# Kernel tuning notes

Measured on AMD Instinct MI355X. Metric: run time of the kernel, lower is better.

Reference implementation:

```python
import jax, jax.numpy as jnp
import numpy as np

COMMITMENT_COST = 0.25
NUM_CODES = 4096
EMBED_DIM = 64


def setup_inputs() -> dict:
    key = jax.random.key(0)
    k1, k2 = jax.random.split(key)
    z_e = jax.random.normal(k1, (65536, EMBED_DIM), dtype=jnp.float32)
    embeddings = jax.random.normal(k2, (NUM_CODES, EMBED_DIM), dtype=jnp.float32)
    return {"z_e": z_e, "embeddings": embeddings}


def reference(z_e, embeddings):
    # Squared Euclidean distances; argmin is identical to torch.cdist argmin.
    # d2[n,k] = |z_e[n]|^2 - 2 z_e[n].e[k] + |e[k]|^2
    z_sq = jnp.sum(z_e * z_e, axis=-1, keepdims=True)            # [N,1]
    e_sq = jnp.sum(embeddings * embeddings, axis=-1)              # [K]
    d2 = z_sq - 2.0 * jnp.einsum('nd,kd->nk', z_e, embeddings) + e_sq  # [N,K]
    indices = jnp.argmin(d2, axis=-1)                             # [N] int
    z_q = embeddings[indices]                                     # [N,D] gather

    # commitment loss = mse(stop_grad(z_q), z_e)
    commitment_loss = COMMITMENT_COST * jnp.mean(
        (jax.lax.stop_gradient(z_q) - z_e) ** 2)

    # straight-through estimator
    z_q_st = z_e + jax.lax.stop_gradient(z_q - z_e)

    # code usage stats: one-hot mean == normalized histogram (scatter-add)
    n = z_e.shape[0]
    counts = jnp.zeros((NUM_CODES,), dtype=jnp.float32).at[indices].add(1.0)
    avg_probs = counts / n
    perplexity = jnp.exp(-jnp.sum(avg_probs * jnp.log(avg_probs + 1e-10)))
    n_active = jnp.sum(avg_probs > 0.001)

    return z_q_st, indices, commitment_loss, perplexity, n_active
```

## Files before the change

### kernel.cpp

```cpp
#include <hip/hip_runtime.h>
#include <math.h>

#define D 64
#define K 4096
#define MARGIN 0.08f
#define KSPLIT 4
#define CPH (K / 16 / KSPLIT)

typedef float f32x4 __attribute__((ext_vector_type(4)));
typedef _Float16 f16x8 __attribute__((ext_vector_type(8)));

__global__ __launch_bounds__(256) void esplit_kernel(const float* __restrict__ emb,
                                                     short* __restrict__ e_h,
                                                     float* __restrict__ e_sq,
                                                     int* __restrict__ counts,
                                                     int* __restrict__ ctrl) {
  int i = blockIdx.x * 256 + threadIdx.x;
  {
    int lane = i & 63;
    int t = (i >> 6) & 1;
    int c = i >> 7;
    int quad = lane >> 4, col = lane & 15;
    const float* src = emb + (size_t)(c * 16 + col) * D + t * 32 + quad * 8;
    f32x4 u0 = *(const f32x4*)src;
    f32x4 u1 = *(const f32x4*)(src + 4);
    f16x8 h;
#pragma unroll
    for (int j = 0; j < 8; ++j) {
      float x = (j < 4) ? u0[j] : u1[j - 4];
      h[j] = (_Float16)x;
    }
    *(f16x8*)(e_h + (size_t)i * 8) = h;
  }
  if (i < 128) ctrl[i] = 0;
  if (i < K) {
    counts[i] = 0;
    const float* e = emb + (size_t)i * D;
    float s = 0.f;
#pragma unroll
    for (int d = 0; d < D; ++d) s = fmaf(e[d], e[d], s);
    e_sq[i] = s;
  }
}

#define MFMA16(A, B, C) __builtin_amdgcn_mfma_f32_16x16x32_f16(A, B, C, 0, 0, 0)

#define STEP(C0, C1, CEQ, N0, N1, NEQ, CC)                                   \
  {                                                                          \
    N0 = *(const f16x8*)(pB);                                                \
    N1 = *(const f16x8*)(pB + 512);                                          \
    NEQ = *pE;                                                               \
    pB += 1024;                                                              \
    pE += 16;                                                                \
    const float seed = -0.5f * (CEQ);                                        \
    f32x4 acc0 = {seed, seed, seed, seed};                                   \
    f32x4 acc1 = {seed, seed, seed, seed};                                   \
    acc0 = MFMA16(a_hi[0][0], C0, acc0);                                     \
    acc1 = MFMA16(a_hi[1][0], C0, acc1);                                     \
    acc0 = MFMA16(a_lo[0][0], C0, acc0);                                     \
    acc1 = MFMA16(a_lo[1][0], C0, acc1);                                     \
    acc0 = MFMA16(a_hi[0][1], C1, acc0);                                     \
    acc1 = MFMA16(a_hi[1][1], C1, acc1);                                     \
    acc0 = MFMA16(a_lo[0][1], C1, acc0);                                     \
    acc1 = MFMA16(a_lo[1][1], C1, acc1);                                     \
    const int cc_ = (CC);                                                    \
    _Pragma("unroll")                                                        \
    for (int r = 0; r < 4; ++r) {                                            \
      float a0 = acc0[r];                                                    \
      float ob = best[r];                                                    \
      best[r] = fmaxf(ob, a0);                                               \
      second[r] = __builtin_amdgcn_fmed3f(ob, a0, second[r]);                \
      bidx[r] = (a0 > ob) ? cc_ : bidx[r];                                   \
    }                                                                        \
    _Pragma("unroll")                                                        \
    for (int r = 0; r < 4; ++r) {                                            \
      float a1 = acc1[r];                                                    \
      float ob = best[4 + r];                                                \
      best[4 + r] = fmaxf(ob, a1);                                           \
      second[4 + r] = __builtin_amdgcn_fmed3f(ob, a1, second[4 + r]);        \
      bidx[4 + r] = (a1 > ob) ? cc_ : bidx[4 + r];                           \
    }                                                                        \
  }

__global__ __launch_bounds__(256, 2) void dist_kernel(const float* __restrict__ z_e,
                                                      const short* __restrict__ e_h,
                                                      const float* __restrict__ esq,
                                                      float* __restrict__ pbest,
                                                      float* __restrict__ psec,
                                                      int* __restrict__ pidx) {
  const int tid = threadIdx.x;
  const int wv = tid >> 6;
  const int lane = tid & 63;
  const int quad = lane >> 4, col = lane & 15;
  const int rowbase = blockIdx.x * 128 + wv * 32;
  const int half = blockIdx.y;
  const int c0 = half * CPH;

  f16x8 a_hi[2][2], a_lo[2][2];
#pragma unroll
  for (int s = 0; s < 2; ++s) {
#pragma unroll
    for (int t = 0; t < 2; ++t) {
      const float* zr = z_e + (size_t)(rowbase + s * 16 + col) * D + t * 32 + quad * 8;
      f32x4 u0 = *(const f32x4*)zr;
      f32x4 u1 = *(const f32x4*)(zr + 4);
#pragma unroll
      for (int j = 0; j < 8; ++j) {
        float x = (j < 4) ? u0[j] : u1[j - 4];
        _Float16 h = (_Float16)x;
        a_hi[s][t][j] = h;
        a_lo[s][t][j] = (_Float16)(x - (float)h);
      }
    }
  }

  float best[8], second[8];
  int bidx[8];
#pragma unroll
  for (int i = 0; i < 8; ++i) {
    best[i] = -__builtin_inff();
    second[i] = -__builtin_inff();
    bidx[i] = 0;
  }

  const short* pB = e_h + (size_t)c0 * 1024 + (size_t)lane * 8;
  const float* pE = esq + c0 * 16 + col;
  f16x8 b0 = *(const f16x8*)pB;
  f16x8 b1 = *(const f16x8*)(pB + 512);
  float eq = *pE;
  pB += 1024;
  pE += 16;
  f16x8 n0, n1;
  float neq;

  for (int cc = 0; cc < CPH; cc += 2) {
    STEP(b0, b1, eq, n0, n1, neq, cc)
    STEP(n0, n1, neq, b0, b1, eq, cc + 1)
  }

#pragma unroll
  for (int i = 0; i < 8; ++i) {
    float b = -2.f * best[i];
    float s2 = -2.f * second[i];
    int ix = (c0 + bidx[i]) * 16 + col;
#pragma unroll
    for (int off = 1; off < 16; off <<= 1) {
      float ob = __shfl_xor(b, off);
      float os = __shfl_xor(s2, off);
      int oi = __shfl_xor(ix, off);
      float ns = fminf(fminf(s2, os), fmaxf(b, ob));
      if (ob < b || (ob == b && oi < ix)) ix = oi;
      b = fminf(b, ob);
      s2 = ns;
    }
    if (col == 0) {
      int row = rowbase + (i >> 2) * 16 + quad * 4 + (i & 3);
      size_t o = (size_t)half * 65536 + row;
      pbest[o] = b;
      psec[o] = s2;
      pidx[o] = ix;
    }
  }
}

__global__ __launch_bounds__(256) void tail_kernel(const float* __restrict__ z_e,
                                                   const float* __restrict__ emb,
                                                   const float* __restrict__ esq,
                                                   const float* __restrict__ pbest,
                                                   const float* __restrict__ psec,
                                                   const int* __restrict__ pidx,
                                                   float* __restrict__ out_zq,
                                                   float* __restrict__ out_idx,
                                                   int* __restrict__ counts,
                                                   int* __restrict__ ctrl,
                                                   float* __restrict__ out_scalars,
                                                   int N) {
  const int tid = threadIdx.x;
  const int wave = tid >> 6;
  const int lane = tid & 63;
  const int base = blockIdx.x * 128;
  int* done = ctrl;
  float* loss_slots = (float*)(ctrl + 8);

  __shared__ int wl[128];
  __shared__ int bidx_s[128];
  __shared__ int wn;
  __shared__ int lastflag;
  __shared__ float zs[4][D];
  __shared__ float se[4];
  __shared__ int sa[4];

  if (tid == 0) wn = 0;
  __syncthreads();

  if (tid < 128) {
    int row = base + tid;
    float b = pbest[row];
    float s2 = psec[row];
    int ix = pidx[row];
#pragma unroll
    for (int h = 1; h < KSPLIT; ++h) {
      size_t o = (size_t)h * 65536 + row;
      float bh = pbest[o];
      float sh = psec[o];
      int ih = pidx[o];
      s2 = fminf(fminf(s2, sh), fmaxf(b, bh));
      if (bh < b) ix = ih;
      b = fminf(b, bh);
    }
    bidx_s[tid] = ix;
    if (s2 - b < MARGIN) {
      int slot = atomicAdd(&wn, 1);
      wl[slot] = row;
    }
  }
  __syncthreads();

  const int n = wn;
  for (int j = wave; j < n; j += 4) {
    const int row = wl[j];
    if (lane < 16) ((f32x4*)zs[wave])[lane] = *((const f32x4*)(z_e + (size_t)row * D) + lane);

    float pb[KSPLIT], ps[KSPLIT];
    int pi[KSPLIT];
    float B = __builtin_inff();
#pragma unroll
    for (int h = 0; h < KSPLIT; ++h) {
      size_t o = (size_t)h * 65536 + row;
      pb[h] = pbest[o];
      ps[h] = psec[o];
      pi[h] = pidx[o];
      B = fminf(B, pb[h]);
    }
    const float lim = B + MARGIN;

    float bv = __builtin_inff();
    int bi = 0;
#pragma unroll
    for (int h = 0; h < KSPLIT; ++h) {
      if (ps[h] < lim) {
        float hb = __builtin_inff();
        int hx = 0;
        for (int t = 0; t < 16; ++t) {
          int c = h * 1024 + t * 64 + lane;
          const f32x4* er = (const f32x4*)(emb + (size_t)c * D);
          f32x4 a = {0.f, 0.f, 0.f, 0.f};
#pragma unroll
          for (int i = 0; i < 16; ++i)
            a = __builtin_elementwise_fma(er[i], ((const f32x4*)zs[wave])[i], a);
          float dot = (a[0] + a[1]) + (a[2] + a[3]);
          float q = fmaf(-2.f, dot, esq[c]);
          if (q < hb) { hb = q; hx = c; }
        }
#pragma unroll
        for (int off = 32; off > 0; off >>= 1) {
          float ov = __shfl_down(hb, off);
          int oi = __shfl_down(hx, off);
          if (ov < hb || (ov == hb && oi < hx)) { hb = ov; hx = oi; }
        }
        hb = __shfl(hb, 0);
        hx = __shfl(hx, 0);
        if (hb < bv || (hb == bv && hx < bi)) { bv = hb; bi = hx; }
      } else if (pb[h] < lim) {
        int c = pi[h];
        float p = emb[(size_t)c * D + lane] * zs[wave][lane];
#pragma unroll
        for (int off = 1; off < 64; off <<= 1) p += __shfl_xor(p, off);
        float q = fmaf(-2.f, p, esq[c]);
        if (q < bv || (q == bv && c < bi)) { bv = q; bi = c; }
      }
    }
    if (lane == 0) bidx_s[row - base] = bi;
  }
  __syncthreads();

  float lloss = 0.f;
  for (int r = wave; r < 128; r += 8) {
    const int r1 = r + 4;
    const int i0 = bidx_s[r];
    const int i1 = bidx_s[r1];
    const size_t row0 = base + r, row1 = base + r1;
    float ze0 = z_e[row0 * D + lane];
    float ze1 = z_e[row1 * D + lane];
    float zq0 = emb[(size_t)i0 * D + lane];
    float zq1 = emb[(size_t)i1 * D + lane];
    out_zq[row0 * D + lane] = ze0 + (zq0 - ze0);
    out_zq[row1 * D + lane] = ze1 + (zq1 - ze1);
    float d0 = zq0 - ze0, d1 = zq1 - ze1;
    lloss = fmaf(d0, d0, lloss);
    lloss = fmaf(d1, d1, lloss);
    if (lane == 0) {
      out_idx[row0] = (float)i0;
      out_idx[row1] = (float)i1;
      atomicAdd(&counts[i0], 1);
      atomicAdd(&counts[i1], 1);
    }
  }
#pragma unroll
  for (int off = 32; off > 0; off >>= 1) lloss += __shfl_down(lloss, off);
  if (lane == 0) atomicAdd(&loss_slots[blockIdx.x & 63], lloss);

  __syncthreads();
  if (tid == 0) {
    __threadfence();
    lastflag = (atomicAdd(done, 1) == (int)gridDim.x - 1);
  }
  __syncthreads();
  if (!lastflag) return;

  float ent = 0.f;
  int act = 0;
  const float invN = 1.0f / (float)N;
  for (int k = tid; k < K; k += 256) {
    float p = (float)atomicAdd(&counts[k], 0) * invN;
    ent += p * logf(p + 1e-10f);
    act += (p > 0.001f) ? 1 : 0;
  }
#pragma unroll
  for (int off = 32; off > 0; off >>= 1) {
    ent += __shfl_down(ent, off);
    act += __shfl_down(act, off);
  }
  if (lane == 0) { se[wave] = ent; sa[wave] = act; }

  float L = 0.f;
  if (wave == 0) {
    L = atomicAdd(&loss_slots[lane], 0.f);
#pragma unroll
    for (int off = 32; off > 0; off >>= 1) L += __shfl_down(L, off);
  }
  __syncthreads();
  if (tid == 0) {
    float E = se[0] + se[1] + se[2] + se[3];
    int A = sa[0] + sa[1] + sa[2] + sa[3];
    out_scalars[0] = 0.25f * L / ((float)N * (float)D);
    out_scalars[1] = expf(-E);
    out_scalars[2] = (float)A;
  }
}

extern "C" void kernel_launch(void* const* d_in, const int* in_sizes, int n_in,
                              void* d_out, int out_size, void* d_ws, size_t ws_size,
                              hipStream_t stream) {
  const float* z_e = (const float*)d_in[0];
  const float* emb = (const float*)d_in[1];
  const int N = in_sizes[0] / D;

  float* out = (float*)d_out;
  float* out_zq = out;
  float* out_idx = out + (size_t)N * D;
  float* out_scalars = out + (size_t)N * (D + 1);

  char* ws = (char*)d_ws;
  size_t o = 0;
  int* counts = (int*)(ws + o);      o += 16384;
  int* ctrl = (int*)(ws + o);        o += 512;
  float* esq = (float*)(ws + o);     o += 16384;
  short* e_h = (short*)(ws + o);     o += (size_t)K * D * 2;
  o += 8192;
  float* pbest = (float*)(ws + o);   o += (size_t)KSPLIT * N * 4;
  float* psec = (float*)(ws + o);    o += (size_t)KSPLIT * N * 4;
  int* pidx = (int*)(ws + o);        o += (size_t)KSPLIT * N * 4;

  esplit_kernel<<<(K / 16) * 2 * 64 / 256, 256, 0, stream>>>(emb, e_h, esq,
                                                             counts, ctrl);
  dist_kernel<<<dim3(N / 128, KSPLIT), 256, 0, stream>>>(z_e, e_h, esq,
                                                         pbest, psec, pidx);
  tail_kernel<<<N / 128, 256, 0, stream>>>(z_e, emb, esq, pbest, psec, pidx,
                                           out_zq, out_idx, counts, ctrl,
                                           out_scalars, N);
}
```

Measured before the change: 235.6 us.

## Stage codebook tiles in LDS with double-buffered global_load_lds

Each wave used to stream its own copy of the fp16 codebook fragments straight from global memory with register prefetch. Now the four waves of a block share a double-buffered LDS tile of 8 code chunks, filled with asynchronous global-to-LDS loads. While one tile is consumed, the next is being loaded, which cuts redundant global and L2 traffic by a factor of four. The cost is a __syncthreads per tile, 32 KB of LDS per block that may limit occupancy, and reliance on correct wait handling for the LDS DMA writes.

```diff
diff --git a/kernel.cpp b/kernel.cpp
--- a/kernel.cpp
+++ b/kernel.cpp
@@ -6,9 +6,16 @@
 #define MARGIN 0.08f
 #define KSPLIT 4
 #define CPH (K / 16 / KSPLIT)
+#define TS 8
+#define NT (CPH / TS)
 
 typedef float f32x4 __attribute__((ext_vector_type(4)));
 typedef _Float16 f16x8 __attribute__((ext_vector_type(8)));
+
+#define GLOAD_LDS(g, l)                                              \
+  __builtin_amdgcn_global_load_lds(                                  \
+      (const __attribute__((address_space(1))) void*)(g),            \
+      (__attribute__((address_space(3))) void*)(l), 16, 0, 0)
 
 __global__ __launch_bounds__(256) void esplit_kernel(const float* __restrict__ emb,
                                                      short* __restrict__ e_h,
@@ -45,43 +52,6 @@
 
 #define MFMA16(A, B, C) __builtin_amdgcn_mfma_f32_16x16x32_f16(A, B, C, 0, 0, 0)
 
-#define STEP(C0, C1, CEQ, N0, N1, NEQ, CC)                                   \
-  {                                                                          \
-    N0 = *(const f16x8*)(pB);                                                \
-    N1 = *(const f16x8*)(pB + 512);                                          \
-    NEQ = *pE;                                                               \
-    pB += 1024;                                                              \
-    pE += 16;                                                                \
-    const float seed = -0.5f * (CEQ);                                        \
-    f32x4 acc0 = {seed, seed, seed, seed};                                   \
-    f32x4 acc1 = {seed, seed, seed, seed};                                   \
-    acc0 = MFMA16(a_hi[0][0], C0, acc0);                                     \
-    acc1 = MFMA16(a_hi[1][0], C0, acc1);                                     \
-    acc0 = MFMA16(a_lo[0][0], C0, acc0);                                     \
-    acc1 = MFMA16(a_lo[1][0], C0, acc1);                                     \
-    acc0 = MFMA16(a_hi[0][1], C1, acc0);                                     \
-    acc1 = MFMA16(a_hi[1][1], C1, acc1);                                     \
-    acc0 = MFMA16(a_lo[0][1], C1, acc0);                                     \
-    acc1 = MFMA16(a_lo[1][1], C1, acc1);                                     \
-    const int cc_ = (CC);                                                    \
-    _Pragma("unroll")                                                        \
-    for (int r = 0; r < 4; ++r) {                                            \
-      float a0 = acc0[r];                                                    \
-      float ob = best[r];                                                    \
-      best[r] = fmaxf(ob, a0);                                               \
-      second[r] = __builtin_amdgcn_fmed3f(ob, a0, second[r]);                \
-      bidx[r] = (a0 > ob) ? cc_ : bidx[r];                                   \
-    }                                                                        \
-    _Pragma("unroll")                                                        \
-    for (int r = 0; r < 4; ++r) {                                            \
-      float a1 = acc1[r];                                                    \
-      float ob = best[4 + r];                                                \
-      best[4 + r] = fmaxf(ob, a1);                                           \
-      second[4 + r] = __builtin_amdgcn_fmed3f(ob, a1, second[4 + r]);        \
-      bidx[4 + r] = (a1 > ob) ? cc_ : bidx[4 + r];                           \
-    }                                                                        \
-  }
-
 __global__ __launch_bounds__(256, 2) void dist_kernel(const float* __restrict__ z_e,
                                                       const short* __restrict__ e_h,
                                                       const float* __restrict__ esq,
@@ -96,6 +66,8 @@
   const int half = blockIdx.y;
   const int c0 = half * CPH;
 
+  __shared__ __align__(16) short sbuf[2 * TS * 1024];
+
   f16x8 a_hi[2][2], a_lo[2][2];
 #pragma unroll
   for (int s = 0; s < 2; ++s) {
@@ -123,19 +95,68 @@
     bidx[i] = 0;
   }
 
-  const short* pB = e_h + (size_t)c0 * 1024 + (size_t)lane * 8;
+  const short* gB = e_h + (size_t)c0 * 1024;
   const float* pE = esq + c0 * 16 + col;
-  f16x8 b0 = *(const f16x8*)pB;
-  f16x8 b1 = *(const f16x8*)(pB + 512);
-  float eq = *pE;
-  pB += 1024;
-  pE += 16;
-  f16x8 n0, n1;
-  float neq;
-
-  for (int cc = 0; cc < CPH; cc += 2) {
-    STEP(b0, b1, eq, n0, n1, neq, cc)
-    STEP(n0, n1, neq, b0, b1, eq, cc + 1)
+
+  {
+    const short* src = gB + (size_t)wv * 2048 + (size_t)lane * 8;
+    short* dst = sbuf + wv * 2048;
+#pragma unroll
+    for (int s = 0; s < 4; ++s) GLOAD_LDS(src + s * 512, dst + s * 512);
+  }
+
+  unsigned rbase = 0;
+  for (int t = 0; t < NT; ++t) {
+    __syncthreads();
+
+    if (t + 1 < NT) {
+      const short* src = gB + (size_t)(t + 1) * (TS * 1024) + wv * 2048 + lane * 8;
+      short* dst = sbuf + (rbase ^ (TS * 1024)) + wv * 2048;
+#pragma unroll
+      for (int s = 0; s < 4; ++s) GLOAD_LDS(src + s * 512, dst + s * 512);
+    }
+
+    float eqt[TS];
+#pragma unroll
+    for (int j = 0; j < TS; ++j) eqt[j] = pE[(t * TS + j) * 16];
+
+    const short* sB = sbuf + rbase;
+#pragma unroll
+    for (int j = 0; j < TS; ++j) {
+      f16x8 b0 = *(const f16x8*)(sB + j * 1024 + lane * 8);
+      f16x8 b1 = *(const f16x8*)(sB + j * 1024 + 512 + lane * 8);
+
+      const float seed = -0.5f * eqt[j];
+      f32x4 acc0 = {seed, seed, seed, seed};
+      f32x4 acc1 = {seed, seed, seed, seed};
+      acc0 = MFMA16(a_hi[0][0], b0, acc0);
+      acc1 = MFMA16(a_hi[1][0], b0, acc1);
+      acc0 = MFMA16(a_lo[0][0], b0, acc0);
+      acc1 = MFMA16(a_lo[1][0], b0, acc1);
+      acc0 = MFMA16(a_hi[0][1], b1, acc0);
+      acc1 = MFMA16(a_hi[1][1], b1, acc1);
+      acc0 = MFMA16(a_lo[0][1], b1, acc0);
+      acc1 = MFMA16(a_lo[1][1], b1, acc1);
+
+      const int cc = t * TS + j;
+#pragma unroll
+      for (int r = 0; r < 4; ++r) {
+        float a0 = acc0[r];
+        float ob = best[r];
+        best[r] = fmaxf(ob, a0);
+        second[r] = __builtin_amdgcn_fmed3f(ob, a0, second[r]);
+        bidx[r] = (a0 > ob) ? cc : bidx[r];
+      }
+#pragma unroll
+      for (int r = 0; r < 4; ++r) {
+        float a1 = acc1[r];
+        float ob = best[4 + r];
+        best[4 + r] = fmaxf(ob, a1);
+        second[4 + r] = __builtin_amdgcn_fmed3f(ob, a1, second[4 + r]);
+        bidx[4 + r] = (a1 > ob) ? cc : bidx[4 + r];
+      }
+    }
+    rbase ^= TS * 1024;
   }
 
 #pragma unroll
```

After: 233.2 us. About the same (-1.0%).
